# Optimization experiments

Measured on AMD Instinct MI355X. Metric: run time of the kernel, lower is better.

Reference implementation:

```python
import jax, jax.numpy as jnp
import numpy as np

X, Y, Z = 38, 24, 24
SCENE_GROUND = np.array([-5.6, -3.6, -2.4], dtype=np.float32)
VOXEL_SIZE = np.array([0.3, 0.3, 0.2], dtype=np.float32)
MIN_VOXEL_COORD = np.floor(SCENE_GROUND / VOXEL_SIZE)  # [-19,-12,-12]

B, C, N = 16, 64, 16384


def setup_inputs() -> dict:
    key = jax.random.key(0)
    k1, k2 = jax.random.split(key)
    features = jax.random.normal(k1, (B, C, N), dtype=jnp.float32)
    # points uniformly inside the voxelized scene box so indices are in range
    lo = jnp.asarray(MIN_VOXEL_COORD * VOXEL_SIZE, dtype=jnp.float32)
    hi = lo + jnp.asarray(np.array([X, Y, Z], np.float32) * VOXEL_SIZE)
    u = jax.random.uniform(k2, (B, N, 3), dtype=jnp.float32)
    coords = lo + u * (hi - lo) * 0.999
    return {"features": features, "coords": coords}


def _voxelize(features, coords):
    # features: [B, C, N], coords: [B, N, 3]
    vs = jnp.asarray(VOXEL_SIZE, dtype=coords.dtype)
    mvc = jnp.asarray(MIN_VOXEL_COORD, dtype=coords.dtype)
    idx = (jnp.floor(coords / vs) - mvc).astype(jnp.int32)  # [B, N, 3]
    dims = jnp.array([X, Y, Z], dtype=jnp.int32)
    valid = jnp.all((idx >= 0) & (idx < dims), axis=-1)  # [B, N]
    R = X * Y * Z
    flat = idx[..., 0] * (Y * Z) + idx[..., 1] * Z + idx[..., 2]  # [B, N]
    flat = jnp.where(valid, flat, R)  # dump out-of-range points into extra segment

    def per_batch(f, seg):
        # f: [C, N], seg: [N]
        sums = jax.ops.segment_sum(f.T, seg, num_segments=R + 1)  # [R+1, C]
        cnts = jax.ops.segment_sum(jnp.ones((f.shape[1],), f.dtype), seg,
                                   num_segments=R + 1)  # [R+1]
        avg = sums / jnp.maximum(cnts, 1.0)[:, None]
        return avg[:R]  # [R, C]

    out = jax.vmap(per_batch)(features, flat)  # [B, R, C]
    out = out.reshape(features.shape[0], X, Y, Z, features.shape[1])
    return jnp.transpose(out, (0, 4, 1, 2, 3))  # [B, C, X, Y, Z]


def reference(features, coords):
    return _voxelize(features, coords)
```

## Files before the change

### kernel.cpp

```cpp
#include <hip/hip_runtime.h>
#include <hip/hip_bf16.h>


#define BB 16
#define CC 64
#define NN 16384
#define XX 38
#define YY 24
#define ZZ 24
#define RR (XX * YY * ZZ)
#define SS 21896
#define RBLK 86
#define NTILES (RR / 64)

__device__ __forceinline__ int voxel_id(const float* __restrict__ coords, int t) {
    float cx = coords[t * 3 + 0];
    float cy = coords[t * 3 + 1];
    float cz = coords[t * 3 + 2];
    int ix = (int)(floorf(cx / 0.3f) + 19.0f);
    int iy = (int)(floorf(cy / 0.3f) + 12.0f);
    int iz = (int)(floorf(cz / 0.2f) + 12.0f);
    bool valid = (ix >= 0) & (ix < XX) & (iy >= 0) & (iy < YY) &
                 (iz >= 0) & (iz < ZZ);
    return valid ? (ix * (YY * ZZ) + iy * ZZ + iz) : RR;
}

__global__ void vox_scatter_t(const float* __restrict__ feat,
                              const float* __restrict__ coords,
                              float* __restrict__ acc,
                              int* __restrict__ cnt) {
    __shared__ float lt[64][65];
    __shared__ int vv[64];
    int blk = blockIdx.x;
    int b = blk >> 8;
    int n0 = (blk & 255) * 64;
    int tid = threadIdx.x;
    int lane = tid & 63, w = tid >> 6;

    if (tid < 64) {
        int v = voxel_id(coords, b * NN + n0 + tid);
        vv[tid] = v;
        if (v < RR) atomicAdd(&cnt[b * RR + v], 1);
    }

    const float* fb = feat + (size_t)b * CC * NN;
#pragma unroll
    for (int it = 0; it < 16; ++it) {
        int c = it * 4 + w;
        lt[lane][c] = fb[(size_t)c * NN + n0 + lane];
    }
    __syncthreads();

#pragma unroll
    for (int i = 0; i < 16; ++i) {
        int p = w * 16 + i;
        int v = vv[p];
        if (v < RR) {
            atomicAdd(&acc[((size_t)b * RR + v) * CC + lane], lt[p][lane]);
        }
    }
}

__global__ void vox_finish(const float* __restrict__ acc,
                           const int* __restrict__ cnt,
                           float* __restrict__ out) {
    __shared__ float lt[64][65];
    int blk = blockIdx.x;
    int b = blk / NTILES;
    int r0 = (blk % NTILES) * 64;
    int tid = threadIdx.x;
    int lane = tid & 63, w = tid >> 6;

#pragma unroll
    for (int i = 0; i < 16; ++i) {
        int rl = w * 16 + i;
        int r = r0 + rl;
        int c_ = cnt[b * RR + r];
        float val = 0.0f;
        if (c_ > 0) {
            val = acc[((size_t)b * RR + r) * CC + lane] / (float)c_;
        }
        lt[rl][lane] = val;
    }
    __syncthreads();

    float* ob = out + (size_t)b * CC * RR;
#pragma unroll
    for (int it = 0; it < 16; ++it) {
        int idx = it * 256 + tid;
        int c = idx >> 6, rr = idx & 63;
        ob[(size_t)c * RR + r0 + rr] = lt[rr][c];
    }
}


__global__ void vox_index_fb(const float* __restrict__ coords,
                             int* __restrict__ hist,
                             int* __restrict__ vid,
                             int* __restrict__ rank) {
    int t = blockIdx.x * blockDim.x + threadIdx.x;
    int b = t >> 14;
    int v = voxel_id(coords, t);
    vid[t] = v;
    rank[t] = atomicAdd(&hist[b * SS + v], 1);
}

__global__ void vox_scan_fb(const int* __restrict__ hist,
                            int* __restrict__ offs) {
    __shared__ int part[256];
    int b = blockIdx.x;
    const int* h = hist + b * SS;
    int* o = offs + b * SS;
    int t = threadIdx.x;
    int base = t * RBLK;
    int end = min(base + RBLK, RR);
    int s = 0;
    for (int i = base; i < end; ++i) s += h[i];
    part[t] = s;
    __syncthreads();
    for (int d = 1; d < 256; d <<= 1) {
        int v = (t >= d) ? part[t - d] : 0;
        __syncthreads();
        part[t] += v;
        __syncthreads();
    }
    int run = (t == 0) ? 0 : part[t - 1];
    for (int i = base; i < end; ++i) {
        o[i] = run;
        run += h[i];
    }
    if (t == 255) o[RR] = part[255];
}

__global__ void vox_sort_fb(const int* __restrict__ vid,
                            const int* __restrict__ rank,
                            const int* __restrict__ offs,
                            int* __restrict__ sidx) {
    int t = blockIdx.x * blockDim.x + threadIdx.x;
    int b = t >> 14;
    int pos = offs[b * SS + vid[t]] + rank[t];
    sidx[b * NN + pos] = t & (NN - 1);
}

__global__ void vox_gather_fb(const float* __restrict__ feat,
                              const int* __restrict__ offs,
                              const int* __restrict__ sidx,
                              float* __restrict__ out) {
    int blk = blockIdx.x;
    int rb = blk % RBLK;
    int bc = blk / RBLK;
    int r = rb * 256 + threadIdx.x;
    if (r >= RR) return;
    int b = bc >> 6;
    const int* o = offs + b * SS;
    int start = o[r], end = o[r + 1];
    const int* si = sidx + b * NN;
    const float* f = feat + (size_t)bc * NN;
    float sum = 0.0f;
    for (int j = start; j < end; ++j) sum += f[si[j]];
    out[(size_t)bc * RR + r] = sum / (float)max(end - start, 1);
}

extern "C" void kernel_launch(void* const* d_in, const int* in_sizes, int n_in,
                              void* d_out, int out_size, void* d_ws, size_t ws_size,
                              hipStream_t stream) {
    const float* feat   = (const float*)d_in[0];
    const float* coords = (const float*)d_in[1];
    float* out = (float*)d_out;

    size_t acc_elems = (size_t)BB * RR * CC;
    size_t cnt_elems = (size_t)BB * RR;
    size_t need_main = (acc_elems + cnt_elems) * 4;
    int pts = BB * NN;

    if (ws_size >= need_main) {
        float* acc = (float*)d_ws;
        int* cnt = (int*)(acc + acc_elems);

        hipMemsetAsync(d_ws, 0, need_main, stream);
        vox_scatter_t<<<BB * (NN / 64), 256, 0, stream>>>(feat, coords, acc, cnt);
        vox_finish<<<BB * NTILES, 256, 0, stream>>>(acc, cnt, out);
    } else {
        int* hist = (int*)d_ws;
        int* offs = hist + BB * SS;
        int* vid  = offs + BB * SS;
        int* rank = vid + BB * NN;
        int* sidx = rank + BB * NN;

        hipMemsetAsync(hist, 0, (size_t)BB * SS * sizeof(int), stream);
        vox_index_fb<<<pts / 256, 256, 0, stream>>>(coords, hist, vid, rank);
        vox_scan_fb<<<BB, 256, 0, stream>>>(hist, offs);
        vox_sort_fb<<<pts / 256, 256, 0, stream>>>(vid, rank, offs, sidx);
        vox_gather_fb<<<BB * CC * RBLK, 256, 0, stream>>>(feat, offs, sidx, out);
    }
}
```

Baseline: 219.3 us.

## Replace atomic scatter with cooperative counting-sort and segmented gather kernel

Adds one cooperative kernel that histograms voxel ids, scans offsets, scatters feature rows into voxel-sorted order, then reduces contiguous segments per voxel and writes the transposed output. This avoids the float atomics into a large zeroed accumulator and the memset of that buffer, replacing them with deterministic sorted sums. In exchange it adds several grid-wide syncs, a serial scan run on only 16 blocks, and a full extra write and read of the features. The older atomic path is kept as a fallback if the cooperative launch fails.

```diff
diff --git a/kernel.cpp b/kernel.cpp
--- a/kernel.cpp
+++ b/kernel.cpp
@@ -1,5 +1,8 @@
 #include <hip/hip_runtime.h>
 #include <hip/hip_bf16.h>
+#include <hip/hip_cooperative_groups.h>
+
+namespace cg = cooperative_groups;
 
 
 #define BB 16
@@ -12,8 +15,9 @@
 #define SS 21896
 #define RBLK 86
 #define NTILES (RR / 64)
-
-__device__ __forceinline__ int voxel_id(const float* __restrict__ coords, int t) {
+#define GRID 1024
+
+__device__ __forceinline__ int voxel_id(const float* coords, int t) {
     float cx = coords[t * 3 + 0];
     float cy = coords[t * 3 + 1];
     float cz = coords[t * 3 + 2];
@@ -24,6 +28,102 @@
                  (iz >= 0) & (iz < ZZ);
     return valid ? (ix * (YY * ZZ) + iy * ZZ + iz) : RR;
 }
+
+__global__ void __launch_bounds__(256, 4)
+vox_coop(const float* feat, const float* coords, float* out,
+         int* hist, int* offs, int* vid, int* rank, float* sfeat) {
+    cg::grid_group grid = cg::this_grid();
+    __shared__ float lt[64][65];
+    __shared__ int ivals[256];
+
+    int bx = blockIdx.x, tid = threadIdx.x;
+    int g = bx * 256 + tid;
+    int lane = tid & 63, w = tid >> 6;
+
+    for (int i = g; i < BB * SS; i += GRID * 256) hist[i] = 0;
+    grid.sync();
+
+    {
+        int b = g >> 14;
+        int v = voxel_id(coords, g);
+        vid[g] = v;
+        rank[g] = atomicAdd(&hist[b * SS + v], 1);
+    }
+    grid.sync();
+
+    if (bx < BB) {
+        const int* h = hist + bx * SS;
+        int* o = offs + bx * SS;
+        int base = tid * RBLK;
+        int end = min(base + RBLK, RR);
+        int s = 0;
+        for (int i = base; i < end; ++i) s += h[i];
+        ivals[tid] = s;
+        __syncthreads();
+        for (int d = 1; d < 256; d <<= 1) {
+            int v2 = (tid >= d) ? ivals[tid - d] : 0;
+            __syncthreads();
+            ivals[tid] += v2;
+            __syncthreads();
+        }
+        int run = (tid == 0) ? 0 : ivals[tid - 1];
+        for (int i = base; i < end; ++i) { o[i] = run; run += h[i]; }
+        if (tid == 255) o[RR] = ivals[255];
+    }
+    grid.sync();
+
+    for (int tile = bx; tile < BB * (NN / 64); tile += GRID) {
+        int b = tile >> 8;
+        int n0 = (tile & 255) * 64;
+        if (tid < 64) {
+            int t = b * NN + n0 + tid;
+            int v = vid[t];
+            ivals[tid] = (v < RR) ? (offs[b * SS + v] + rank[t]) : -1;
+        }
+        const float* fb = feat + (size_t)b * CC * NN;
+#pragma unroll
+        for (int it = 0; it < 16; ++it) {
+            int c = it * 4 + w;
+            lt[lane][c] = fb[(size_t)c * NN + n0 + lane];
+        }
+        __syncthreads();
+        float* sb = sfeat + (size_t)b * NN * CC;
+#pragma unroll
+        for (int i = 0; i < 16; ++i) {
+            int p = w * 16 + i;
+            int dst = ivals[p];
+            if (dst >= 0) sb[(size_t)dst * CC + lane] = lt[p][lane];
+        }
+        __syncthreads();
+    }
+    grid.sync();
+
+    for (int tile = bx; tile < BB * NTILES; tile += GRID) {
+        int b = tile / NTILES;
+        int r0 = (tile % NTILES) * 64;
+        const int* o = offs + b * SS;
+        const float* sb = sfeat + (size_t)b * NN * CC;
+#pragma unroll
+        for (int i = 0; i < 16; ++i) {
+            int rl = w * 16 + i;
+            int r = r0 + rl;
+            int s2 = o[r], e2 = o[r + 1];
+            float sum = 0.0f;
+            for (int j = s2; j < e2; ++j) sum += sb[(size_t)j * CC + lane];
+            lt[rl][lane] = sum / (float)max(e2 - s2, 1);
+        }
+        __syncthreads();
+        float* ob = out + (size_t)b * CC * RR;
+#pragma unroll
+        for (int it = 0; it < 16; ++it) {
+            int idx = it * 256 + tid;
+            int c = idx >> 6, rr = idx & 63;
+            ob[(size_t)c * RR + r0 + rr] = lt[rr][c];
+        }
+        __syncthreads();
+    }
+}
+
 
 __global__ void vox_scatter_t(const float* __restrict__ feat,
                               const float* __restrict__ coords,
@@ -36,13 +136,11 @@
     int n0 = (blk & 255) * 64;
     int tid = threadIdx.x;
     int lane = tid & 63, w = tid >> 6;
-
     if (tid < 64) {
         int v = voxel_id(coords, b * NN + n0 + tid);
         vv[tid] = v;
         if (v < RR) atomicAdd(&cnt[b * RR + v], 1);
     }
-
     const float* fb = feat + (size_t)b * CC * NN;
 #pragma unroll
     for (int it = 0; it < 16; ++it) {
@@ -50,14 +148,11 @@
         lt[lane][c] = fb[(size_t)c * NN + n0 + lane];
     }
     __syncthreads();
-
 #pragma unroll
     for (int i = 0; i < 16; ++i) {
         int p = w * 16 + i;
         int v = vv[p];
-        if (v < RR) {
-            atomicAdd(&acc[((size_t)b * RR + v) * CC + lane], lt[p][lane]);
-        }
+        if (v < RR) atomicAdd(&acc[((size_t)b * RR + v) * CC + lane], lt[p][lane]);
     }
 }
 
@@ -70,20 +165,16 @@
     int r0 = (blk % NTILES) * 64;
     int tid = threadIdx.x;
     int lane = tid & 63, w = tid >> 6;
-
 #pragma unroll
     for (int i = 0; i < 16; ++i) {
         int rl = w * 16 + i;
         int r = r0 + rl;
         int c_ = cnt[b * RR + r];
         float val = 0.0f;
-        if (c_ > 0) {
-            val = acc[((size_t)b * RR + r) * CC + lane] / (float)c_;
-        }
+        if (c_ > 0) val = acc[((size_t)b * RR + r) * CC + lane] / (float)c_;
         lt[rl][lane] = val;
     }
     __syncthreads();
-
     float* ob = out + (size_t)b * CC * RR;
 #pragma unroll
     for (int it = 0; it < 16; ++it) {
@@ -96,13 +187,13 @@
 
 __global__ void vox_index_fb(const float* __restrict__ coords,
                              int* __restrict__ hist,
-                             int* __restrict__ vid,
-                             int* __restrict__ rank) {
+                             int* __restrict__ vidp,
+                             int* __restrict__ rankp) {
     int t = blockIdx.x * blockDim.x + threadIdx.x;
     int b = t >> 14;
     int v = voxel_id(coords, t);
-    vid[t] = v;
-    rank[t] = atomicAdd(&hist[b * SS + v], 1);
+    vidp[t] = v;
+    rankp[t] = atomicAdd(&hist[b * SS + v], 1);
 }
 
 __global__ void vox_scan_fb(const int* __restrict__ hist,
@@ -125,20 +216,17 @@
         __syncthreads();
     }
     int run = (t == 0) ? 0 : part[t - 1];
-    for (int i = base; i < end; ++i) {
-        o[i] = run;
-        run += h[i];
-    }
+    for (int i = base; i < end; ++i) { o[i] = run; run += h[i]; }
     if (t == 255) o[RR] = part[255];
 }
 
-__global__ void vox_sort_fb(const int* __restrict__ vid,
-                            const int* __restrict__ rank,
+__global__ void vox_sort_fb(const int* __restrict__ vidp,
+                            const int* __restrict__ rankp,
                             const int* __restrict__ offs,
                             int* __restrict__ sidx) {
     int t = blockIdx.x * blockDim.x + threadIdx.x;
     int b = t >> 14;
-    int pos = offs[b * SS + vid[t]] + rank[t];
+    int pos = offs[b * SS + vidp[t]] + rankp[t];
     sidx[b * NN + pos] = t & (NN - 1);
 }
 
@@ -167,27 +255,41 @@
     const float* feat   = (const float*)d_in[0];
     const float* coords = (const float*)d_in[1];
     float* out = (float*)d_out;
+    int pts = BB * NN;
+
+    size_t ss = (size_t)BB * SS;
+    size_t ints = 2 * ss + 2 * (size_t)pts;
+    size_t need_coop = ints * 4 + (size_t)BB * NN * CC * 4;
+
+    if (ws_size >= need_coop) {
+        int* hist  = (int*)d_ws;
+        int* offs  = hist + ss;
+        int* vid   = offs + ss;
+        int* rank  = vid + pts;
+        float* sfeat = (float*)(rank + pts);
+        void* args[] = { (void*)&feat, (void*)&coords, (void*)&out,
+                         (void*)&hist, (void*)&offs, (void*)&vid,
+                         (void*)&rank, (void*)&sfeat };
+        hipError_t err = hipLaunchCooperativeKernel(
+            (void*)vox_coop, dim3(GRID), dim3(256), args, 0, stream);
+        if (err == hipSuccess) return;
+    }
 
     size_t acc_elems = (size_t)BB * RR * CC;
-    size_t cnt_elems = (size_t)BB * RR;
-    size_t need_main = (acc_elems + cnt_elems) * 4;
-    int pts = BB * NN;
-
-    if (ws_size >= need_main) {
+    size_t need_atomic = (acc_elems + (size_t)BB * RR) * 4;
+    if (ws_size >= need_atomic) {
         float* acc = (float*)d_ws;
         int* cnt = (int*)(acc + acc_elems);
-
-        hipMemsetAsync(d_ws, 0, need_main, stream);
+        hipMemsetAsync(d_ws, 0, need_atomic, stream);
         vox_scatter_t<<<BB * (NN / 64), 256, 0, stream>>>(feat, coords, acc, cnt);
         vox_finish<<<BB * NTILES, 256, 0, stream>>>(acc, cnt, out);
     } else {
         int* hist = (int*)d_ws;
-        int* offs = hist + BB * SS;
-        int* vid  = offs + BB * SS;
-        int* rank = vid + BB * NN;
-        int* sidx = rank + BB * NN;
-
-        hipMemsetAsync(hist, 0, (size_t)BB * SS * sizeof(int), stream);
+        int* offs = hist + ss;
+        int* vid  = offs + ss;
+        int* rank = vid + pts;
+        int* sidx = rank + pts;
+        hipMemsetAsync(hist, 0, ss * sizeof(int), stream);
         vox_index_fb<<<pts / 256, 256, 0, stream>>>(coords, hist, vid, rank);
         vox_scan_fb<<<BB, 256, 0, stream>>>(hist, offs);
         vox_sort_fb<<<pts / 256, 256, 0, stream>>>(vid, rank, offs, sidx);
```

Result: slower. 696.2 us (+217.4%).
